# Performance work log

Measured on AMD Instinct MI355X. Metric: run time of the kernel, lower is better.

The kernel has to match this reference:

```python
import jax, jax.numpy as jnp
from jax import lax
import numpy as np

CODE_DIM = 256
CODE_SIZE = 1024
BETA = 0.25


def _conv2d(x, w, b, stride, pad):
    # x: NCHW, w: OIHW (pytorch Conv2d layout)
    y = lax.conv_general_dilated(x, w, (stride, stride), [(pad, pad), (pad, pad)],
                                 dimension_numbers=('NCHW', 'OIHW', 'NCHW'))
    return y + b[None, :, None, None]


def _conv_transpose2d(x, w, b, stride, pad):
    # w: pytorch ConvTranspose2d layout [in, out, kh, kw]
    kh, kw = w.shape[2], w.shape[3]
    wf = jnp.flip(w, (2, 3)).transpose(1, 0, 2, 3)  # -> OIHW with spatial flip
    y = lax.conv_general_dilated(x, wf, (1, 1),
                                 [(kh - 1 - pad, kh - 1 - pad), (kw - 1 - pad, kw - 1 - pad)],
                                 lhs_dilation=(stride, stride),
                                 dimension_numbers=('NCHW', 'OIHW', 'NCHW'))
    return y + b[None, :, None, None]


def setup_inputs() -> dict:
    key = jax.random.key(0)
    ks = jax.random.split(key, 14)
    f32 = jnp.float32

    def p(k, shape, s=0.05):
        return jax.random.normal(k, shape, f32) * s

    return {
        'x': jax.random.normal(ks[0], (64, 1, 128, 128), f32),
        'enc_w1': p(ks[1], (64, 1, 5, 5)), 'enc_b1': jnp.zeros((64,), f32),
        'enc_w2': p(ks[2], (64, 64, 5, 5)), 'enc_b2': jnp.zeros((64,), f32),
        'enc_w3': p(ks[3], (CODE_DIM, 64, 5, 5)), 'enc_b3': jnp.zeros((CODE_DIM,), f32),
        'codebook': p(ks[4], (CODE_SIZE, CODE_DIM)),
        'dec_w1': p(ks[5], (CODE_DIM, 64, 4, 4)), 'dec_b1': jnp.zeros((64,), f32),
        'dec_w2': p(ks[6], (64, 64, 4, 4)), 'dec_b2': jnp.zeros((64,), f32),
        'dec_w3': p(ks[7], (1, 64, 3, 3)), 'dec_b3': jnp.zeros((1,), f32),
    }


def reference(x, enc_w1, enc_b1, enc_w2, enc_b2, enc_w3, enc_b3, codebook,
              dec_w1, dec_b1, dec_w2, dec_b2, dec_w3, dec_b3):
    # ---- encoder ----
    z = jax.nn.relu(_conv2d(x, enc_w1, enc_b1, 2, 2))
    z = jax.nn.relu(_conv2d(z, enc_w2, enc_b2, 1, 2))
    z = _conv2d(z, enc_w3, enc_b3, 2, 2)  # [B, D, H/4, W/4]

    # ---- quantize (eval mode: no EMA buffer updates) ----
    b, c, h, w = z.shape
    flat = z.transpose(0, 2, 3, 1).reshape(-1, c)  # [BHW, D]
    # ||z||^2 - 2 z.W^T + ||w||^2
    dists = ((flat ** 2).sum(axis=1, keepdims=True)
             - 2.0 * flat @ codebook.T
             + (codebook ** 2).sum(axis=1)[None, :])  # [BHW, K]
    idx = jnp.argmin(dists, axis=1)
    e = codebook[idx].reshape(b, h, w, c).transpose(0, 3, 1, 2)  # [B, D, h, w]
    e_st = lax.stop_gradient(e - z) + z  # straight-through

    # ---- decoder ----
    y = jax.nn.relu(_conv_transpose2d(e_st, dec_w1, dec_b1, 2, 1))
    y = jax.nn.relu(_conv_transpose2d(y, dec_w2, dec_b2, 2, 1))
    x_tilde = jnp.tanh(_conv2d(y, dec_w3, dec_b3, 1, 1))

    diff = jnp.mean((z - lax.stop_gradient(e)) ** 2)
    return x_tilde, diff
```

## Files before the change

kernel.cpp:

```cpp
#include <hip/hip_runtime.h>

typedef _Float16 f16;
typedef _Float16 f16x8 __attribute__((ext_vector_type(8)));
typedef _Float16 f16x4 __attribute__((ext_vector_type(4)));
typedef _Float16 h2 __attribute__((ext_vector_type(2)));
typedef float f32x4 __attribute__((ext_vector_type(4)));
typedef unsigned short u16;
typedef unsigned int u32;

#define DEVI __device__ __forceinline__

DEVI u16 f2h(float f) { f16 h = (f16)f; return __builtin_bit_cast(u16, h); }
DEVI float h2f(u16 u) { f16 h = __builtin_bit_cast(f16, u); return (float)h; }

__launch_bounds__(256)
__global__ void prep_wconv_k(const float* __restrict__ src, u16* __restrict__ dst, int nf_sh) {
    int i = blockIdx.x * 256 + threadIdx.x;
    int j = i & 7, lane = (i >> 3) & 63;
    int q = i >> 9;
    int f = q & ((1 << nf_sh) - 1); q >>= nf_sh;
    int pl = q & 1; q >>= 1;
    int icc = q & 1; int tap = q >> 1;
    int oc = (f << 4) + (lane & 15);
    int ic = icc * 32 + ((lane >> 4) << 3) + j;
    float w = src[(oc * 64 + ic) * 25 + tap];
    if (pl == 0) dst[i] = f2h(w);
    else         dst[i] = f2h((w - h2f(f2h(w))) * 4096.f);
}
__launch_bounds__(256)
__global__ void prep_wdec_k(const float* __restrict__ src, u16* __restrict__ dst, int icc_sh) {
    int i = blockIdx.x * 256 + threadIdx.x;
    int j = i & 7, lane = (i >> 3) & 63;
    int f = (i >> 9) & 3;
    int q = i >> 11;
    int icc = q & ((1 << icc_sh) - 1); int tap = q >> icc_sh;
    int oc = (f << 4) + (lane & 15);
    int ic = icc * 32 + ((lane >> 4) << 3) + j;
    dst[i] = f2h(src[(ic * 64 + oc) * 16 + tap]);
}
__launch_bounds__(256)
__global__ void prep_cb_k(const float* __restrict__ cb, u16* __restrict__ dst) {
    int i = blockIdx.x * 256 + threadIdx.x;
    int j = i & 7, lane = (i >> 3) & 63;
    int f = (i >> 9) & 63;
    int q = i >> 15;
    int pl = q & 1; int ks = q >> 1;
    int n = (f << 4) + (lane & 15);
    int k = ks * 32 + ((lane >> 4) << 3) + j;
    float w = cb[n * 256 + k];
    if (pl == 0) dst[i] = f2h(w);
    else         dst[i] = f2h((w - h2f(f2h(w))) * 4096.f);
}
__launch_bounds__(256)
__global__ void prep_cbn_k(const float* __restrict__ cb, float* __restrict__ cbn) {
    int row = blockIdx.x * 256 + threadIdx.x;
    float s = 0.f;
    for (int c = 0; c < 256; c += 4) {
        f32x4 v = *(const f32x4*)&cb[row * 256 + c];
        s = fmaf(v.x, v.x, s); s = fmaf(v.y, v.y, s);
        s = fmaf(v.z, v.z, s); s = fmaf(v.w, v.w, s);
    }
    cbn[row] = s;
}

__launch_bounds__(256)
__global__ void conv1_k(const float* __restrict__ x, const float* __restrict__ w,
                        const float* __restrict__ b, u16* __restrict__ oh, u16* __restrict__ ol) {
    __shared__ float wl[25 * 64];
    __shared__ float bl[64];
    int t = threadIdx.x;
    for (int i = t; i < 1600; i += 256) wl[(i % 25) * 64 + i / 25] = w[i];
    if (t < 64) bl[t] = b[t];
    __syncthreads();
    int p = blockIdx.x * 256 + t;
    int ox = p & 63, oy = (p >> 6) & 63, n = p >> 12;
    f32x4 acc[16];
    #pragma unroll
    for (int c = 0; c < 16; ++c) acc[c] = *(f32x4*)&bl[c * 4];
    for (int dy = 0; dy < 5; ++dy) {
        int iy = 2 * oy - 2 + dy;
        if ((unsigned)iy >= 128u) continue;
        for (int dx = 0; dx < 5; ++dx) {
            int ix = 2 * ox - 2 + dx;
            if ((unsigned)ix >= 128u) continue;
            float v = x[(n * 128 + iy) * 128 + ix];
            const float* wp = &wl[(dy * 5 + dx) * 64];
            #pragma unroll
            for (int c = 0; c < 16; ++c) {
                f32x4 w4 = *(const f32x4*)&wp[c * 4];
                acc[c].x = fmaf(v, w4.x, acc[c].x); acc[c].y = fmaf(v, w4.y, acc[c].y);
                acc[c].z = fmaf(v, w4.z, acc[c].z); acc[c].w = fmaf(v, w4.w, acc[c].w);
            }
        }
    }
    #pragma unroll
    for (int c = 0; c < 16; ++c) {
        ushort4 uh, ul;
        float vv[4] = {acc[c].x, acc[c].y, acc[c].z, acc[c].w};
        u16 rh[4], rl[4];
        #pragma unroll
        for (int k = 0; k < 4; ++k) {
            float v = fmaxf(vv[k], 0.f);
            f16 hh = (f16)v;
            rh[k] = __builtin_bit_cast(u16, hh);
            rl[k] = f2h((v - (float)hh) * 4096.f);
        }
        uh.x = rh[0]; uh.y = rh[1]; uh.z = rh[2]; uh.w = rh[3];
        ul.x = rl[0]; ul.y = rl[1]; ul.z = rl[2]; ul.w = rl[3];
        *(ushort4*)&oh[p * 64 + c * 4] = uh;
        *(ushort4*)&ol[p * 64 + c * 4] = ul;
    }
}

__launch_bounds__(256, 2)
__global__ void conv5w_k(const u16* __restrict__ Ah_g, const u16* __restrict__ Al_g,
                         const u16* __restrict__ wBf, const float* __restrict__ bias,
                         u16* __restrict__ Oh, u16* __restrict__ Ol) {
    constexpr int PATCH = 20;
    constexpr int NPIX = PATCH * PATCH;
    constexpr int PLSZ = (NPIX / 2) * 64;
    __shared__ u16 patch[2 * PLSZ];

    int t = threadIdx.x, l = t & 63, wv = t >> 6, g = l >> 4;
    int qy = wv >> 1, qx = wv & 1;

    int bi = blockIdx.x;
    int wlin = (bi & 7) * ((int)gridDim.x >> 3) + (bi >> 3);
    int txi = wlin & 3; int rest = wlin >> 2;
    int tyi = rest & 3; int n = rest >> 2;
    int iy0 = (tyi << 4) - 2, ix0 = (txi << 4) - 2;

    int ppb[4];
    #pragma unroll
    for (int mi = 0; mi < 4; ++mi) {
        int m = mi * 16 + (l & 15);
        ppb[mi] = ((qy << 3) + (m >> 3)) * PATCH + (qx << 3) + (m & 7);
    }

    f32x4 acc0[4][4], acc1[4][4];
    f32x4 z4 = {0.f, 0.f, 0.f, 0.f};
    #pragma unroll
    for (int mi = 0; mi < 4; ++mi)
        #pragma unroll
        for (int ni = 0; ni < 4; ++ni) { acc0[mi][ni] = z4; acc1[mi][ni] = z4; }

    int tap0 = bi % 25;
    int dy0 = tap0 / 5, dx0 = tap0 - 5 * dy0;
    int tadd0 = dy0 * PATCH + dx0;
    int iccr = bi & 1;
    const size_t tstride = 16 * 512;

    for (int icci = 0; icci < 2; ++icci) {
        int icc = icci ^ iccr;
        __syncthreads();
        for (int i = t; i < NPIX * 8; i += 256) {
            int c = i & 3; int r2 = i >> 2;
            int pl = (r2 >= NPIX); int pp = r2 - pl * NPIX;
            int py = pp / PATCH, px = pp - py * PATCH;
            int iy = iy0 + py, ix = ix0 + px;
            uint4 v = make_uint4(0u, 0u, 0u, 0u);
            if ((unsigned)iy < 64u && (unsigned)ix < 64u)
                v = *(const uint4*)&(pl ? Al_g : Ah_g)[(((n * 64 + iy) * 64 + ix)) * 64 + icc * 32 + c * 8];
            int P = pp >> 1, r = pp & 1;
            int slot = (r << 2) | ((c + P) & 3);
            *(uint4*)&patch[pl * PLSZ + (P << 6) + (slot << 3)] = v;
        }
        __syncthreads();

        const u16* pB = wBf + (size_t)((tap0 * 4 + icc * 2) * 4) * 512 + l * 8;
        int tap = tap0, dx = dx0, tadd = tadd0;
        for (int tapi = 0; tapi < 25; ++tapi) {
            f16x8 Bh[4], Bl[4];
            #pragma unroll
            for (int ni = 0; ni < 4; ++ni) {
                Bh[ni] = *(const f16x8*)&pB[ni * 512];
                Bl[ni] = *(const f16x8*)&pB[(4 + ni) * 512];
            }
            #pragma unroll
            for (int mi = 0; mi < 4; ++mi) {
                int pp = ppb[mi] + tadd;
                int P = pp >> 1, r = pp & 1;
                int offs = (P << 6) + (((r << 2) | ((g + P) & 3)) << 3);
                f16x8 ah = *(const f16x8*)&patch[offs];
                f16x8 al = *(const f16x8*)&patch[PLSZ + offs];
                #pragma unroll
                for (int ni = 0; ni < 4; ++ni) {
                    acc0[mi][ni] = __builtin_amdgcn_mfma_f32_16x16x32_f16(ah, Bh[ni], acc0[mi][ni], 0, 0, 0);
                    acc1[mi][ni] = __builtin_amdgcn_mfma_f32_16x16x32_f16(ah, Bl[ni], acc1[mi][ni], 0, 0, 0);
                    acc1[mi][ni] = __builtin_amdgcn_mfma_f32_16x16x32_f16(al, Bh[ni], acc1[mi][ni], 0, 0, 0);
                }
            }
            pB = (tap == 24) ? (pB - 24 * tstride) : (pB + tstride);
            if (tap == 24) { tap = 0; dx = 0; tadd = 0; }
            else {
                tap++; dx++; tadd++;
                if (dx == 5) { dx = 0; tadd += PATCH - 5; }
            }
        }
    }
    #pragma unroll
    for (int mi = 0; mi < 4; ++mi)
        #pragma unroll
        for (int ni = 0; ni < 4; ++ni) {
            int oc = ni * 16 + (l & 15);
            float bv = bias[oc];
            #pragma unroll
            for (int reg = 0; reg < 4; ++reg) {
                float v = acc0[mi][ni][reg] + acc1[mi][ni][reg] * (1.f / 4096.f) + bv;
                v = fmaxf(v, 0.f);
                int pix = mi * 16 + g * 4 + reg;
                int oy = (tyi << 4) + (qy << 3) + (pix >> 3);
                int ox = (txi << 4) + (qx << 3) + (pix & 7);
                int idx = ((n * 64 + oy) * 64 + ox) * 64 + oc;
                f16 hh = (f16)v;
                Oh[idx] = __builtin_bit_cast(u16, hh);
                Ol[idx] = f2h((v - (float)hh) * 4096.f);
            }
        }
}

template<int S, int OCT, int NI, bool RELU>
__launch_bounds__(256)
__global__ void conv5_k(const u16* __restrict__ Ah_g, const u16* __restrict__ Al_g,
                        const u16* __restrict__ wBf, const float* __restrict__ bias,
                        u16* __restrict__ Oh, u16* __restrict__ Ol,
                        int IH, int IW, int OH, int OW) {
    constexpr int PATCH = 7 * S + 5;
    constexpr int NPIX = PATCH * PATCH;
    constexpr int NPAIR = (NPIX + 1) / 2;
    constexpr int PLSZ = NPAIR * 64;
    constexpr int NF = OCT / 16;
    constexpr int OCB = OCT / (NI * 64);
    __shared__ u16 patch[2 * PLSZ];

    int t = threadIdx.x, l = t & 63, wv = t >> 6, g = l >> 4;

    int bi = blockIdx.x;
    int wlin = (bi & 7) * ((int)gridDim.x >> 3) + (bi >> 3);
    int ocb = wlin % OCB; int rest = wlin / OCB;
    int tw = OW >> 3, th = OH >> 3;
    int txi = rest % tw; rest /= tw;
    int tyi = rest % th; int n = rest / th;
    int iy0 = S * (tyi << 3) - 2, ix0 = S * (txi << 3) - 2;

    int ppb[4];
    #pragma unroll
    for (int mi = 0; mi < 4; ++mi) {
        int m = mi * 16 + (l & 15);
        ppb[mi] = (S * (m >> 3)) * PATCH + S * (m & 7);
    }

    f32x4 acc0[4][NI], acc1[4][NI];
    f32x4 z4 = {0.f, 0.f, 0.f, 0.f};
    #pragma unroll
    for (int mi = 0; mi < 4; ++mi)
        #pragma unroll
        for (int ni = 0; ni < NI; ++ni) { acc0[mi][ni] = z4; acc1[mi][ni] = z4; }

    int tap0 = bi % 25;
    int dy0 = tap0 / 5, dx0 = tap0 - 5 * dy0;
    int tadd0 = dy0 * PATCH + dx0;
    int iccr = bi & 1;
    int fg = ocb * (4 * NI) + wv * NI;
    const size_t tstride = (size_t)(4 * NF) * 512;

    for (int icci = 0; icci < 2; ++icci) {
        int icc = icci ^ iccr;
        __syncthreads();
        for (int i = t; i < NPIX * 8; i += 256) {
            int c = i & 3; int r2 = i >> 2;
            int pl = (r2 >= NPIX); int pp = r2 - pl * NPIX;
            int py = pp / PATCH, px = pp - py * PATCH;
            int iy = iy0 + py, ix = ix0 + px;
            uint4 v = make_uint4(0u, 0u, 0u, 0u);
            if ((unsigned)iy < (unsigned)IH && (unsigned)ix < (unsigned)IW)
                v = *(const uint4*)&(pl ? Al_g : Ah_g)[(((n * IH + iy) * IW + ix)) * 64 + icc * 32 + c * 8];
            int P = pp >> 1, r = pp & 1;
            *(uint4*)&patch[pl * PLSZ + (P << 6) + (((P + (c << 1) + r) & 7) << 3)] = v;
        }
        __syncthreads();

        const u16* pB = wBf + (size_t)((tap0 * 4 + icc * 2) * NF + fg) * 512 + l * 8;
        int tap = tap0, dx = dx0, tadd = tadd0;
        for (int tapi = 0; tapi < 25; ++tapi) {
            f16x8 Bh[NI], Bl[NI];
            #pragma unroll
            for (int ni = 0; ni < NI; ++ni) {
                Bh[ni] = *(const f16x8*)&pB[ni * 512];
                Bl[ni] = *(const f16x8*)&pB[(NF + ni) * 512];
            }
            f16x8 ah[4], al[4];
            #pragma unroll
            for (int mi = 0; mi < 4; ++mi) {
                int pp = ppb[mi] + tadd;
                int P = pp >> 1, r = pp & 1;
                int offs = (P << 6) + (((P + (g << 1) + r) & 7) << 3);
                ah[mi] = *(const f16x8*)&patch[offs];
                al[mi] = *(const f16x8*)&patch[PLSZ + offs];
            }
            #pragma unroll
            for (int mi = 0; mi < 4; ++mi)
                #pragma unroll
                for (int ni = 0; ni < NI; ++ni) {
                    acc0[mi][ni] = __builtin_amdgcn_mfma_f32_16x16x32_f16(ah[mi], Bh[ni], acc0[mi][ni], 0, 0, 0);
                    acc1[mi][ni] = __builtin_amdgcn_mfma_f32_16x16x32_f16(ah[mi], Bl[ni], acc1[mi][ni], 0, 0, 0);
                    acc1[mi][ni] = __builtin_amdgcn_mfma_f32_16x16x32_f16(al[mi], Bh[ni], acc1[mi][ni], 0, 0, 0);
                }
            pB = (tap == 24) ? (pB - 24 * tstride) : (pB + tstride);
            if (tap == 24) { tap = 0; dx = 0; tadd = 0; }
            else {
                tap++; dx++; tadd++;
                if (dx == 5) { dx = 0; tadd += PATCH - 5; }
            }
        }
    }
    #pragma unroll
    for (int mi = 0; mi < 4; ++mi)
        #pragma unroll
        for (int ni = 0; ni < NI; ++ni) {
            int oc = (fg + ni) * 16 + (l & 15);
            float bv = bias[oc];
            #pragma unroll
            for (int reg = 0; reg < 4; ++reg) {
                float v = acc0[mi][ni][reg] + acc1[mi][ni][reg] * (1.f / 4096.f) + bv;
                if (RELU) v = fmaxf(v, 0.f);
                int pix = mi * 16 + g * 4 + reg;
                int oy = (tyi << 3) + (pix >> 3), ox = (txi << 3) + (pix & 7);
                int idx = ((n * OH + oy) * OW + ox) * OCT + oc;
                f16 hh = (f16)v;
                Oh[idx] = __builtin_bit_cast(u16, hh);
                Ol[idx] = f2h((v - (float)hh) * 4096.f);
            }
        }
}

__launch_bounds__(256, 2)
__global__ void quant_k(const u16* __restrict__ zh, const u16* __restrict__ zl,
                        const u16* __restrict__ cbf, const float* __restrict__ cbn,
                        const float* __restrict__ cb, u16* __restrict__ e,
                        float* __restrict__ diff) {
    __shared__ u16 Bbuf[2 * 32 * 512];
    __shared__ float cbn_l[1024];
    __shared__ float zn_l[128];
    __shared__ float bd_l[128];
    __shared__ int   wi_l[128];

    int t = threadIdx.x, l = t & 63, wv = t >> 6, g = l >> 4;
    int bi = blockIdx.x;
    int row0 = bi << 7;

    {
        f32x4 v = *(const f32x4*)&cbn[t * 4];
        *(f32x4*)&cbn_l[t * 4] = v;
    }

    f16x8 Ah[2][8], Al[2][8];
    int rbase = row0 + wv * 32 + (l & 15);
    #pragma unroll
    for (int mi = 0; mi < 2; ++mi)
        #pragma unroll
        for (int ks = 0; ks < 8; ++ks) {
            size_t off = (size_t)(rbase + mi * 16) * 256 + ks * 32 + g * 8;
            Ah[mi][ks] = *(const f16x8*)&zh[off];
            Al[mi][ks] = *(const f16x8*)&zl[off];
        }

    #pragma unroll
    for (int mi = 0; mi < 2; ++mi) {
        float s = 0.f;
        #pragma unroll
        for (int ks = 0; ks < 8; ++ks)
            #pragma unroll
            for (int j = 0; j < 8; ++j) {
                float v = (float)Ah[mi][ks][j] + (float)Al[mi][ks][j] * (1.f / 4096.f);
                s = fmaf(v, v, s);
            }
        s += __shfl_xor(s, 16);
        s += __shfl_xor(s, 32);
        if (g == 0) zn_l[wv * 32 + mi * 16 + (l & 15)] = s;
    }

    float rd[8]; int rc[8];
    #pragma unroll
    for (int s = 0; s < 8; ++s) { rd[s] = 1e30f; rc[s] = 0; }

    int fi = wv * 8;
    {
        int no0 = bi & 31;
        #pragma unroll
        for (int q = 0; q < 8; ++q) {
            int f2 = fi + q;
            int ks = f2 >> 2, pl = (f2 >> 1) & 1, nf = f2 & 1;
            f16x8 v = *(const f16x8*)&cbf[(size_t)(((ks * 2 + pl) * 64) + no0 * 2 + nf) * 512 + l * 8];
            *(uint4*)&Bbuf[(size_t)f2 * 512 + l * 8] = __builtin_bit_cast(uint4, v);
        }
    }
    __syncthreads();

    for (int noi = 0; noi < 32; ++noi) {
        int b = noi & 1;
        int no_cur = (noi + bi) & 31;

        f16x8 pf[8];
        if (noi < 31) {
            int no_n = (noi + 1 + bi) & 31;
            #pragma unroll
            for (int q = 0; q < 8; ++q) {
                int f2 = fi + q;
                int ks = f2 >> 2, pl = (f2 >> 1) & 1, nf = f2 & 1;
                pf[q] = *(const f16x8*)&cbf[(size_t)(((ks * 2 + pl) * 64) + no_n * 2 + nf) * 512 + l * 8];
            }
        }

        f32x4 acc0[2][2], acc1[2][2];
        f32x4 z4 = {0.f, 0.f, 0.f, 0.f};
        #pragma unroll
        for (int mi = 0; mi < 2; ++mi)
            #pragma unroll
            for (int nf = 0; nf < 2; ++nf) { acc0[mi][nf] = z4; acc1[mi][nf] = z4; }

        #pragma unroll
        for (int ks = 0; ks < 8; ++ks) {
            const u16* bb = &Bbuf[(size_t)(b * 32 + ks * 4) * 512 + l * 8];
            f16x8 Bh0 = *(const f16x8*)&bb[0 * 512];
            f16x8 Bh1 = *(const f16x8*)&bb[1 * 512];
            f16x8 Bl0 = *(const f16x8*)&bb[2 * 512];
            f16x8 Bl1 = *(const f16x8*)&bb[3 * 512];
            #pragma unroll
            for (int mi = 0; mi < 2; ++mi) {
                acc0[mi][0] = __builtin_amdgcn_mfma_f32_16x16x32_f16(Ah[mi][ks], Bh0, acc0[mi][0], 0, 0, 0);
                acc0[mi][1] = __builtin_amdgcn_mfma_f32_16x16x32_f16(Ah[mi][ks], Bh1, acc0[mi][1], 0, 0, 0);
                acc1[mi][0] = __builtin_amdgcn_mfma_f32_16x16x32_f16(Ah[mi][ks], Bl0, acc1[mi][0], 0, 0, 0);
                acc1[mi][0] = __builtin_amdgcn_mfma_f32_16x16x32_f16(Al[mi][ks], Bh0, acc1[mi][0], 0, 0, 0);
                acc1[mi][1] = __builtin_amdgcn_mfma_f32_16x16x32_f16(Ah[mi][ks], Bl1, acc1[mi][1], 0, 0, 0);
                acc1[mi][1] = __builtin_amdgcn_mfma_f32_16x16x32_f16(Al[mi][ks], Bh1, acc1[mi][1], 0, 0, 0);
            }
        }

        #pragma unroll
        for (int nf = 0; nf < 2; ++nf) {
            int col = no_cur * 32 + nf * 16 + (l & 15);
            float cn = cbn_l[col];
            #pragma unroll
            for (int mi = 0; mi < 2; ++mi)
                #pragma unroll
                for (int reg = 0; reg < 4; ++reg) {
                    float d = cn - 2.f * (acc0[mi][nf][reg] + acc1[mi][nf][reg] * (1.f / 4096.f));
                    int slot = mi * 4 + reg;
                    if (d < rd[slot] || (d == rd[slot] && col < rc[slot])) { rd[slot] = d; rc[slot] = col; }
                }
        }

        if (noi < 31) {
            #pragma unroll
            for (int q = 0; q < 8; ++q)
                *(uint4*)&Bbuf[(size_t)((1 - b) * 32 + fi + q) * 512 + l * 8] = __builtin_bit_cast(uint4, pf[q]);
        }
        __syncthreads();
    }

    #pragma unroll
    for (int step = 1; step < 16; step <<= 1) {
        #pragma unroll
        for (int s = 0; s < 8; ++s) {
            float od = __shfl_xor(rd[s], step);
            int ocl = __shfl_xor(rc[s], step);
            if (od < rd[s] || (od == rd[s] && ocl < rc[s])) { rd[s] = od; rc[s] = ocl; }
        }
    }
    if ((l & 15) == 0) {
        #pragma unroll
        for (int s = 0; s < 8; ++s) {
            int mi = s >> 2, reg = s & 3;
            int row = wv * 32 + mi * 16 + g * 4 + reg;
            bd_l[row] = rd[s]; wi_l[row] = rc[s];
        }
    }
    __syncthreads();
    if (t < 64) {
        float dval = (zn_l[t] + bd_l[t]) + (zn_l[t + 64] + bd_l[t + 64]);
        #pragma unroll
        for (int step = 1; step < 64; step <<= 1) dval += __shfl_xor(dval, step);
        if (t == 0) atomicAdd(diff, dval * (1.f / 16777216.f));
    }
    __syncthreads();
    for (int r = 0; r < 128; ++r) {
        int wi = wi_l[r];
        e[(size_t)(row0 + r) * 256 + t] = f2h(cb[wi * 256 + t]);
    }
}

template<int ICT>
__launch_bounds__(256)
__global__ void deconv4_k(const u16* __restrict__ in, const u16* __restrict__ wdf,
                          const float* __restrict__ bias, u16* __restrict__ out,
                          int IH, int IW) {
    constexpr int RST = 40;
    constexpr int ICC = ICT / 32;
    constexpr int PLSZ = 81 * RST;
    __shared__ u16 patch[PLSZ];

    int t = threadIdx.x, l = t & 63, wv = t >> 6;
    int wm = wv >> 1, wn = wv & 1, g = l >> 4;

    int bi = blockIdx.x;
    int wlin = (bi & 7) * ((int)gridDim.x >> 3) + (bi >> 3);
    int par = wlin & 3; int ry = par >> 1, rx = par & 1;
    int rest = wlin >> 2;
    int tw = IW >> 3, th = IH >> 3;
    int txi = rest % tw; rest /= tw;
    int tyi = rest % th; int n = rest / th;
    int a0 = tyi << 3, b0 = txi << 3;
    int by0 = ry ? 0 : -1, bx0 = rx ? 0 : -1;
    int OH = IH << 1, OW = IW << 1;

    int pb0[2];
    #pragma unroll
    for (int mi = 0; mi < 2; ++mi) {
        int m = wm * 32 + mi * 16 + (l & 15);
        int pa = m >> 3, pb_ = m & 7;
        pb0[mi] = (pa * 9 + pb_) * RST + g * 8;
    }

    f32x4 acc[2][2];
    f32x4 z4 = {0.f, 0.f, 0.f, 0.f};
    #pragma unroll
    for (int mi = 0; mi < 2; ++mi)
        #pragma unroll
        for (int ni = 0; ni < 2; ++ni) acc[mi][ni] = z4;

    auto ldB = [&](int icc, int tt, f16x8* B) {
        int tty = tt >> 1, ttx = tt & 1;
        int ky = 1 - ry + 2 * tty, kx = 1 - rx + 2 * ttx;
        int tap = ky * 4 + kx;
        #pragma unroll
        for (int ni = 0; ni < 2; ++ni)
            B[ni] = *(const f16x8*)&wdf[(size_t)((tap * ICC + icc) * 4 + wn * 2 + ni) * 512 + l * 8];
    };

    f16x8 B0[2], B1[2];
    {
        int icc0 = (bi >> 2) & (ICC - 1);
        ldB(icc0, bi & 3, B0);
    }

    for (int icci = 0; icci < ICC; ++icci) {
        int icc = (icci + (bi >> 2)) & (ICC - 1);
        __syncthreads();
        for (int i = t; i < 324; i += 256) {
            int c = i & 3; int pp = i >> 2;
            int pr = pp / 9, pc = pp - pr * 9;
            int ar = a0 + by0 + pr, ac = b0 + bx0 + pc;
            uint4 v = make_uint4(0u, 0u, 0u, 0u);
            if ((unsigned)ar < (unsigned)IH && (unsigned)ac < (unsigned)IW)
                v = *(const uint4*)&in[((n * IH + ar) * IW + ac) * ICT + icc * 32 + c * 8];
            *(uint4*)&patch[(pr * 9 + pc) * RST + c * 8] = v;
        }
        __syncthreads();
        #pragma unroll
        for (int tti = 0; tti < 4; ++tti) {
            int tt = (tti + bi) & 3;
            if (!(icci == ICC - 1 && tti == 3)) {
                int nicci = (tti == 3) ? icci + 1 : icci;
                int ntti = (tti == 3) ? 0 : tti + 1;
                int nicc = (nicci + (bi >> 2)) & (ICC - 1);
                ldB(nicc, (ntti + bi) & 3, B1);
            }
            int tty = tt >> 1, ttx = tt & 1;
            int shift = ((1 - tty) * 9 + (1 - ttx)) * RST;
            #pragma unroll
            for (int mi = 0; mi < 2; ++mi) {
                f16x8 a = *(const f16x8*)&patch[pb0[mi] + shift];
                #pragma unroll
                for (int ni = 0; ni < 2; ++ni)
                    acc[mi][ni] = __builtin_amdgcn_mfma_f32_16x16x32_f16(a, B0[ni], acc[mi][ni], 0, 0, 0);
            }
            B0[0] = B1[0]; B0[1] = B1[1];
        }
    }
    #pragma unroll
    for (int mi = 0; mi < 2; ++mi)
        #pragma unroll
        for (int ni = 0; ni < 2; ++ni) {
            int oc = wn * 32 + ni * 16 + (l & 15);
            float bv = bias[oc];
            #pragma unroll
            for (int reg = 0; reg < 4; ++reg) {
                float v = fmaxf(acc[mi][ni][reg] + bv, 0.f);
                int pix = wm * 32 + mi * 16 + g * 4 + reg;
                int oy = ((a0 + (pix >> 3)) << 1) + ry;
                int ox = ((b0 + (pix & 7)) << 1) + rx;
                out[((n * OH + oy) * OW + ox) * 64 + oc] = f2h(v);
            }
        }
}

__launch_bounds__(256)
__global__ void conv3x3_tanh_k(const u16* __restrict__ in, const float* __restrict__ w,
                               const float* __restrict__ b, float* __restrict__ out) {
    __shared__ u16 tile[18 * 18 * 72];
    __shared__ u32 wpk[288];
    int t = threadIdx.x;
    int bi = blockIdx.x;
    int wlin = (bi & 7) * ((int)gridDim.x >> 3) + (bi >> 3);
    int n = wlin >> 6;
    int tile6 = wlin & 63;
    int ty0 = (tile6 >> 3) << 4, tx0 = (tile6 & 7) << 4;

    for (int i = t; i < 288; i += 256) {
        int tap = i >> 5, icp = i & 31;
        h2 p;
        p.x = (f16)w[(2 * icp) * 9 + tap];
        p.y = (f16)w[(2 * icp + 1) * 9 + tap];
        wpk[tap * 32 + icp] = __builtin_bit_cast(u32, p);
    }
    for (int i = t; i < 2592; i += 256) {
        int ch = i & 7, pix = i >> 3;
        int pr = pix / 18, pc = pix - pr * 18;
        int gy = ty0 - 1 + pr, gx = tx0 - 1 + pc;
        uint4 v = make_uint4(0u, 0u, 0u, 0u);
        if ((unsigned)gy < 128u && (unsigned)gx < 128u)
            v = *(const uint4*)&in[(((n << 7) + gy) * 128 + gx) * 64 + ch * 8];
        *(uint4*)&tile[pix * 72 + ch * 8] = v;
    }
    __syncthreads();

    int ty = t >> 4, tx = t & 15;
    float acc = b[0];
    #pragma unroll
    for (int dy = 0; dy < 3; ++dy) {
        #pragma unroll
        for (int dx = 0; dx < 3; ++dx) {
            int base = ((ty + dy) * 18 + (tx + dx)) * 72;
            const u32* wp = &wpk[(dy * 3 + dx) * 32];
            #pragma unroll
            for (int c8 = 0; c8 < 8; ++c8) {
                uint4 v = *(const uint4*)&tile[base + c8 * 8];
                acc = __builtin_amdgcn_fdot2(__builtin_bit_cast(h2, v.x),
                        __builtin_bit_cast(h2, wp[c8 * 4 + 0]), acc, false);
                acc = __builtin_amdgcn_fdot2(__builtin_bit_cast(h2, v.y),
                        __builtin_bit_cast(h2, wp[c8 * 4 + 1]), acc, false);
                acc = __builtin_amdgcn_fdot2(__builtin_bit_cast(h2, v.z),
                        __builtin_bit_cast(h2, wp[c8 * 4 + 2]), acc, false);
                acc = __builtin_amdgcn_fdot2(__builtin_bit_cast(h2, v.w),
                        __builtin_bit_cast(h2, wp[c8 * 4 + 3]), acc, false);
            }
        }
    }
    int oy = ty0 + ty, ox = tx0 + tx;
    out[(n << 14) + (oy << 7) + ox] = tanhf(acc);
}

extern "C" void kernel_launch(void* const* d_in, const int* in_sizes, int n_in,
                              void* d_out, int out_size, void* d_ws, size_t ws_size,
                              hipStream_t stream) {
    (void)in_sizes; (void)n_in; (void)out_size; (void)ws_size;
    const float* x   = (const float*)d_in[0];
    const float* ew1 = (const float*)d_in[1];
    const float* eb1 = (const float*)d_in[2];
    const float* ew2 = (const float*)d_in[3];
    const float* eb2 = (const float*)d_in[4];
    const float* ew3 = (const float*)d_in[5];
    const float* eb3 = (const float*)d_in[6];
    const float* cb  = (const float*)d_in[7];
    const float* dw1 = (const float*)d_in[8];
    const float* db1 = (const float*)d_in[9];
    const float* dw2 = (const float*)d_in[10];
    const float* db2 = (const float*)d_in[11];
    const float* dw3 = (const float*)d_in[12];
    const float* db3 = (const float*)d_in[13];
    float* out = (float*)d_out;

    u16* ws = (u16*)d_ws;
    u16* a1h = ws;             u16* a1l = ws + 16777216;
    u16* zh  = ws;             u16* zl  = ws + 16777216;
    u16* a2h = ws + 33554432;  u16* a2l = ws + 50331648;
    u16* e   = ws + 33554432;
    u16* y1  = ws + 67108864;
    u16* y2  = ws;
    u16* wBf2 = ws + 83886080;
    u16* wBf3 = wBf2 + 204800;
    u16* wd1f = wBf3 + 819200;
    u16* wd2f = wd1f + 262144;
    u16* cbf  = wd2f + 65536;
    float* cbn = (float*)(cbf + 524288);

    hipMemsetAsync(out + 1048576, 0, 4, stream);

    prep_wconv_k<<<800, 256, 0, stream>>>(ew2, wBf2, 2);
    prep_wconv_k<<<3200, 256, 0, stream>>>(ew3, wBf3, 4);
    prep_wdec_k<<<1024, 256, 0, stream>>>(dw1, wd1f, 3);
    prep_wdec_k<<<256, 256, 0, stream>>>(dw2, wd2f, 1);
    prep_cb_k<<<2048, 256, 0, stream>>>(cb, cbf);
    prep_cbn_k<<<4, 256, 0, stream>>>(cb, cbn);

    conv1_k<<<1024, 256, 0, stream>>>(x, ew1, eb1, a1h, a1l);
    conv5w_k<<<1024, 256, 0, stream>>>(a1h, a1l, wBf2, eb2, a2h, a2l);
    conv5_k<2, 256, 2, false><<<2048, 256, 0, stream>>>(a2h, a2l, wBf3, eb3, zh, zl, 64, 64, 32, 32);
    quant_k<<<512, 256, 0, stream>>>(zh, zl, cbf, cbn, cb, e, out + 1048576);
    deconv4_k<256><<<4096, 256, 0, stream>>>(e, wd1f, db1, y1, 32, 32);
    deconv4_k<64><<<16384, 256, 0, stream>>>(y1, wd2f, db2, y2, 64, 64);
    conv3x3_tanh_k<<<4096, 256, 0, stream>>>(y2, dw3, db3, out);
}
```

Before: 658.1 us.

## Retile third encoder conv so each block covers all 256 output channels

```diff
diff --git a/kernel.cpp b/kernel.cpp
--- a/kernel.cpp
+++ b/kernel.cpp
@@ -12,6 +12,8 @@
 
 DEVI u16 f2h(float f) { f16 h = (f16)f; return __builtin_bit_cast(u16, h); }
 DEVI float h2f(u16 u) { f16 h = __builtin_bit_cast(f16, u); return (float)h; }
+
+DEVI int slotf(int P, int c, int r) { return ((c + P) & 3) | (((r + (P >> 2)) & 1) << 2); }
 
 __launch_bounds__(256)
 __global__ void prep_wconv_k(const float* __restrict__ src, u16* __restrict__ dst, int nf_sh) {
@@ -219,49 +221,45 @@
         }
 }
 
-template<int S, int OCT, int NI, bool RELU>
-__launch_bounds__(256)
-__global__ void conv5_k(const u16* __restrict__ Ah_g, const u16* __restrict__ Al_g,
-                        const u16* __restrict__ wBf, const float* __restrict__ bias,
-                        u16* __restrict__ Oh, u16* __restrict__ Ol,
-                        int IH, int IW, int OH, int OW) {
-    constexpr int PATCH = 7 * S + 5;
+__launch_bounds__(256, 2)
+__global__ void conv5x_k(const u16* __restrict__ Ah_g, const u16* __restrict__ Al_g,
+                         const u16* __restrict__ wBf, const float* __restrict__ bias,
+                         u16* __restrict__ Oh, u16* __restrict__ Ol) {
+    constexpr int PATCH = 19;
     constexpr int NPIX = PATCH * PATCH;
     constexpr int NPAIR = (NPIX + 1) / 2;
     constexpr int PLSZ = NPAIR * 64;
-    constexpr int NF = OCT / 16;
-    constexpr int OCB = OCT / (NI * 64);
+    constexpr int NF = 16;
     __shared__ u16 patch[2 * PLSZ];
 
     int t = threadIdx.x, l = t & 63, wv = t >> 6, g = l >> 4;
+    int wy = wv >> 1, wx = wv & 1;
 
     int bi = blockIdx.x;
     int wlin = (bi & 7) * ((int)gridDim.x >> 3) + (bi >> 3);
-    int ocb = wlin % OCB; int rest = wlin / OCB;
-    int tw = OW >> 3, th = OH >> 3;
-    int txi = rest % tw; rest /= tw;
-    int tyi = rest % th; int n = rest / th;
-    int iy0 = S * (tyi << 3) - 2, ix0 = S * (txi << 3) - 2;
-
-    int ppb[4];
-    #pragma unroll
-    for (int mi = 0; mi < 4; ++mi) {
-        int m = mi * 16 + (l & 15);
-        ppb[mi] = (S * (m >> 3)) * PATCH + S * (m & 7);
-    }
-
-    f32x4 acc0[4][NI], acc1[4][NI];
+    int txi = wlin & 3; int rest = wlin >> 2;
+    int tyi = rest & 3; int n = rest >> 2;
+    int iy0 = ((tyi << 3) << 1) - 2, ix0 = ((txi << 3) << 1) - 2;
+
+    int ppb[2];
+    #pragma unroll
+    for (int mi = 0; mi < 2; ++mi) {
+        int m = wy * 32 + mi * 16 + (l & 15);
+        ppb[mi] = (2 * (m >> 3)) * PATCH + 2 * (m & 7);
+    }
+
+    f32x4 acc0[2][8], acc1[2][8];
     f32x4 z4 = {0.f, 0.f, 0.f, 0.f};
     #pragma unroll
-    for (int mi = 0; mi < 4; ++mi)
-        #pragma unroll
-        for (int ni = 0; ni < NI; ++ni) { acc0[mi][ni] = z4; acc1[mi][ni] = z4; }
+    for (int mi = 0; mi < 2; ++mi)
+        #pragma unroll
+        for (int ni = 0; ni < 8; ++ni) { acc0[mi][ni] = z4; acc1[mi][ni] = z4; }
 
     int tap0 = bi % 25;
     int dy0 = tap0 / 5, dx0 = tap0 - 5 * dy0;
     int tadd0 = dy0 * PATCH + dx0;
     int iccr = bi & 1;
-    int fg = ocb * (4 * NI) + wv * NI;
+    int fg = wx * 8;
     const size_t tstride = (size_t)(4 * NF) * 512;
 
     for (int icci = 0; icci < 2; ++icci) {
@@ -273,39 +271,43 @@
             int py = pp / PATCH, px = pp - py * PATCH;
             int iy = iy0 + py, ix = ix0 + px;
             uint4 v = make_uint4(0u, 0u, 0u, 0u);
-            if ((unsigned)iy < (unsigned)IH && (unsigned)ix < (unsigned)IW)
-                v = *(const uint4*)&(pl ? Al_g : Ah_g)[(((n * IH + iy) * IW + ix)) * 64 + icc * 32 + c * 8];
+            if ((unsigned)iy < 64u && (unsigned)ix < 64u)
+                v = *(const uint4*)&(pl ? Al_g : Ah_g)[(((n * 64 + iy) * 64 + ix)) * 64 + icc * 32 + c * 8];
             int P = pp >> 1, r = pp & 1;
-            *(uint4*)&patch[pl * PLSZ + (P << 6) + (((P + (c << 1) + r) & 7) << 3)] = v;
+            *(uint4*)&patch[pl * PLSZ + (P << 6) + (slotf(P, c, r) << 3)] = v;
         }
         __syncthreads();
 
         const u16* pB = wBf + (size_t)((tap0 * 4 + icc * 2) * NF + fg) * 512 + l * 8;
         int tap = tap0, dx = dx0, tadd = tadd0;
         for (int tapi = 0; tapi < 25; ++tapi) {
-            f16x8 Bh[NI], Bl[NI];
-            #pragma unroll
-            for (int ni = 0; ni < NI; ++ni) {
-                Bh[ni] = *(const f16x8*)&pB[ni * 512];
-                Bl[ni] = *(const f16x8*)&pB[(NF + ni) * 512];
-            }
-            f16x8 ah[4], al[4];
-            #pragma unroll
-            for (int mi = 0; mi < 4; ++mi) {
+            f16x8 ah[2], al[2];
+            #pragma unroll
+            for (int mi = 0; mi < 2; ++mi) {
                 int pp = ppb[mi] + tadd;
                 int P = pp >> 1, r = pp & 1;
-                int offs = (P << 6) + (((P + (g << 1) + r) & 7) << 3);
+                int offs = (P << 6) + (slotf(P, g, r) << 3);
                 ah[mi] = *(const f16x8*)&patch[offs];
                 al[mi] = *(const f16x8*)&patch[PLSZ + offs];
             }
             #pragma unroll
-            for (int mi = 0; mi < 4; ++mi)
+            for (int nc = 0; nc < 2; ++nc) {
+                f16x8 Bh[4], Bl[4];
                 #pragma unroll
-                for (int ni = 0; ni < NI; ++ni) {
-                    acc0[mi][ni] = __builtin_amdgcn_mfma_f32_16x16x32_f16(ah[mi], Bh[ni], acc0[mi][ni], 0, 0, 0);
-                    acc1[mi][ni] = __builtin_amdgcn_mfma_f32_16x16x32_f16(ah[mi], Bl[ni], acc1[mi][ni], 0, 0, 0);
-                    acc1[mi][ni] = __builtin_amdgcn_mfma_f32_16x16x32_f16(al[mi], Bh[ni], acc1[mi][ni], 0, 0, 0);
+                for (int k = 0; k < 4; ++k) {
+                    Bh[k] = *(const f16x8*)&pB[(nc * 4 + k) * 512];
+                    Bl[k] = *(const f16x8*)&pB[(NF + nc * 4 + k) * 512];
                 }
+                #pragma unroll
+                for (int mi = 0; mi < 2; ++mi)
+                    #pragma unroll
+                    for (int k = 0; k < 4; ++k) {
+                        int ni = nc * 4 + k;
+                        acc0[mi][ni] = __builtin_amdgcn_mfma_f32_16x16x32_f16(ah[mi], Bh[k], acc0[mi][ni], 0, 0, 0);
+                        acc1[mi][ni] = __builtin_amdgcn_mfma_f32_16x16x32_f16(ah[mi], Bl[k], acc1[mi][ni], 0, 0, 0);
+                        acc1[mi][ni] = __builtin_amdgcn_mfma_f32_16x16x32_f16(al[mi], Bh[k], acc1[mi][ni], 0, 0, 0);
+                    }
+            }
             pB = (tap == 24) ? (pB - 24 * tstride) : (pB + tstride);
             if (tap == 24) { tap = 0; dx = 0; tadd = 0; }
             else {
@@ -315,18 +317,17 @@
         }
     }
     #pragma unroll
-    for (int mi = 0; mi < 4; ++mi)
-        #pragma unroll
-        for (int ni = 0; ni < NI; ++ni) {
+    for (int mi = 0; mi < 2; ++mi)
+        #pragma unroll
+        for (int ni = 0; ni < 8; ++ni) {
             int oc = (fg + ni) * 16 + (l & 15);
             float bv = bias[oc];
             #pragma unroll
             for (int reg = 0; reg < 4; ++reg) {
                 float v = acc0[mi][ni][reg] + acc1[mi][ni][reg] * (1.f / 4096.f) + bv;
-                if (RELU) v = fmaxf(v, 0.f);
-                int pix = mi * 16 + g * 4 + reg;
+                int pix = wy * 32 + mi * 16 + g * 4 + reg;
                 int oy = (tyi << 3) + (pix >> 3), ox = (txi << 3) + (pix & 7);
-                int idx = ((n * OH + oy) * OW + ox) * OCT + oc;
+                int idx = ((n * 32 + oy) * 32 + ox) * 256 + oc;
                 f16 hh = (f16)v;
                 Oh[idx] = __builtin_bit_cast(u16, hh);
                 Ol[idx] = f2h((v - (float)hh) * 4096.f);
@@ -696,7 +697,7 @@
 
     conv1_k<<<1024, 256, 0, stream>>>(x, ew1, eb1, a1h, a1l);
     conv5w_k<<<1024, 256, 0, stream>>>(a1h, a1l, wBf2, eb2, a2h, a2l);
-    conv5_k<2, 256, 2, false><<<2048, 256, 0, stream>>>(a2h, a2l, wBf3, eb3, zh, zl, 64, 64, 32, 32);
+    conv5x_k<<<1024, 256, 0, stream>>>(a2h, a2l, wBf3, eb3, zh, zl);
     quant_k<<<512, 256, 0, stream>>>(zh, zl, cbf, cbn, cb, e, out + 1048576);
     deconv4_k<256><<<4096, 256, 0, stream>>>(e, wd1f, db1, y1, 32, 32);
     deconv4_k<64><<<16384, 256, 0, stream>>>(y1, wd2f, db2, y2, 64, 64);
```

Result: no change. 656.2 us (-0.3%).
